# Optimization experiments

Measured on AMD Instinct MI355X. Metric: run time of the kernel, lower is better.

## Reference

```python
import jax, jax.numpy as jnp
import numpy as np

N_EMBD = 1024
N_HEAD = 16
HEAD_SIZE = N_EMBD // N_HEAD
EPS = 1e-5


def layernorm(x, g, b):
    mu = jnp.mean(x, axis=-1, keepdims=True)
    var = jnp.var(x, axis=-1, keepdims=True)
    return (x - mu) * jax.lax.rsqrt(var + EPS) * g + b


def setup_inputs() -> dict:
    key = jax.random.key(0)
    ks = jax.random.split(key, 12)
    s = 0.02
    C = N_EMBD
    return {
        "x": jax.random.normal(ks[0], (2, 2048, C), dtype=jnp.float32),
        "Wq": jax.random.normal(ks[1], (C, C), dtype=jnp.float32) * s,
        "Wk": jax.random.normal(ks[2], (C, C), dtype=jnp.float32) * s,
        "Wv": jax.random.normal(ks[3], (C, C), dtype=jnp.float32) * s,
        "Wo": jax.random.normal(ks[4], (C, C), dtype=jnp.float32) * s,
        "bo": jnp.zeros((C,), dtype=jnp.float32),
        "W1": jax.random.normal(ks[5], (C, 4 * C), dtype=jnp.float32) * s,
        "b1": jnp.zeros((4 * C,), dtype=jnp.float32),
        "W2": jax.random.normal(ks[6], (4 * C, C), dtype=jnp.float32) * s,
        "b2": jnp.zeros((C,), dtype=jnp.float32),
        "ln1_g": jnp.ones((C,), dtype=jnp.float32),
        "ln1_b": jnp.zeros((C,), dtype=jnp.float32),
        "ln2_g": jnp.ones((C,), dtype=jnp.float32),
        "ln2_b": jnp.zeros((C,), dtype=jnp.float32),
    }


def reference(x, Wq, Wk, Wv, Wo, bo, W1, b1, W2, b2, ln1_g, ln1_b, ln2_g, ln2_b):
    B, T, C = x.shape
    H, Dh = N_HEAD, HEAD_SIZE

    # --- self-attention branch ---
    h = layernorm(x, ln1_g, ln1_b)
    q = (h @ Wq).reshape(B, T, H, Dh)
    k = (h @ Wk).reshape(B, T, H, Dh)
    v = (h @ Wv).reshape(B, T, H, Dh)

    # NOTE: original scales by C**-0.5 (n_embd), not head_size**-0.5
    scale = C ** (-0.5)
    scores = jnp.einsum("bqhd,bkhd->bhqk", q, k) * scale  # [B,H,T,T]
    causal = jnp.tril(jnp.ones((T, T), dtype=bool))
    scores = jnp.where(causal, scores, -jnp.inf)
    wei = jax.nn.softmax(scores, axis=-1)
    attn = jnp.einsum("bhqk,bkhd->bqhd", wei, v).reshape(B, T, C)
    x = x + attn @ Wo + bo

    # --- MLP branch ---
    h2 = layernorm(x, ln2_g, ln2_b)
    ff = jax.nn.relu(h2 @ W1 + b1) @ W2 + b2
    return x + ff
```

## Files before the change

### kernel.cpp

```cpp
#include <hip/hip_runtime.h>

typedef unsigned short u16;
typedef __bf16 bf16;
typedef bf16 bf16x8 __attribute__((ext_vector_type(8)));
typedef float f32x4 __attribute__((ext_vector_type(4)));


__device__ __forceinline__ u16 f2bf(float f) {
  bf16 b = (bf16)f;
  return __builtin_bit_cast(u16, b);
}

__device__ __forceinline__ void gll16(void* lds, const void* g) {
  __builtin_amdgcn_global_load_lds((__attribute__((address_space(1))) void*)g,
                                   (__attribute__((address_space(3))) void*)lds,
                                   16, 0, 0);
}

__device__ __forceinline__ f32x4 mfma16(bf16x8 a, bf16x8 b, f32x4 c) {
  return __builtin_amdgcn_mfma_f32_16x16x32_bf16(a, b, c, 0, 0, 0);
}


__global__ __launch_bounds__(256)
void transpose_all(const float* __restrict__ Wq, const float* __restrict__ Wk,
                   const float* __restrict__ Wv, const float* __restrict__ Wo,
                   const float* __restrict__ W1, const float* __restrict__ W2,
                   u16* __restrict__ WqT, u16* __restrict__ WkT,
                   u16* __restrict__ WvT, u16* __restrict__ WoT,
                   u16* __restrict__ W1T, u16* __restrict__ W2T) {
  __shared__ float tile[32][33];
  const int id = blockIdx.x;
  const float* src;
  u16* dst;
  int R, C, t;
  if (id < 4096) {
    const int w = id >> 10;
    t = id & 1023; R = 1024; C = 1024;
    src = w == 0 ? Wq : w == 1 ? Wk : w == 2 ? Wv : Wo;
    dst = w == 0 ? WqT : w == 1 ? WkT : w == 2 ? WvT : WoT;
  } else if (id < 8192) {
    t = id - 4096; R = 1024; C = 4096; src = W1; dst = W1T;
  } else {
    t = id - 8192; R = 4096; C = 1024; src = W2; dst = W2T;
  }
  const int tilesx = C >> 5;
  const int c0 = (t % tilesx) * 32, r0 = (t / tilesx) * 32;
  const int tx = threadIdx.x, ty = threadIdx.y;
#pragma unroll
  for (int i = 0; i < 4; ++i)
    tile[ty + i * 8][tx] = src[(size_t)(r0 + ty + i * 8) * C + c0 + tx];
  __syncthreads();
#pragma unroll
  for (int i = 0; i < 4; ++i)
    dst[(size_t)(c0 + ty + i * 8) * R + r0 + tx] = f2bf(tile[tx][ty + i * 8]);
}


__global__ __launch_bounds__(256)
void ln_kernel(const float* __restrict__ x, const float* __restrict__ g,
               const float* __restrict__ bb, u16* __restrict__ h) {
  const int row = blockIdx.x;
  const int tid = threadIdx.x;
  const float4 xv = ((const float4*)(x + (size_t)row * 1024))[tid];
  float s = xv.x + xv.y + xv.z + xv.w;
  float q = xv.x * xv.x + xv.y * xv.y + xv.z * xv.z + xv.w * xv.w;
#pragma unroll
  for (int m = 1; m < 64; m <<= 1) {
    s += __shfl_xor(s, m);
    q += __shfl_xor(q, m);
  }
  __shared__ float ss[4], qq[4];
  const int wid = tid >> 6, lane = tid & 63;
  if (lane == 0) { ss[wid] = s; qq[wid] = q; }
  __syncthreads();
  s = ss[0] + ss[1] + ss[2] + ss[3];
  q = qq[0] + qq[1] + qq[2] + qq[3];
  const float mean = s * (1.0f / 1024.0f);
  const float var = q * (1.0f / 1024.0f) - mean * mean;
  const float rs = rsqrtf(var + 1e-5f);
  const float4 gv = ((const float4*)g)[tid];
  const float4 bv = ((const float4*)bb)[tid];
  ushort4 o;
  o.x = f2bf((xv.x - mean) * rs * gv.x + bv.x);
  o.y = f2bf((xv.y - mean) * rs * gv.y + bv.y);
  o.z = f2bf((xv.z - mean) * rs * gv.z + bv.z);
  o.w = f2bf((xv.w - mean) * rs * gv.w + bv.w);
  ((ushort4*)(h + (size_t)row * 1024))[tid] = o;
}


__device__ __forceinline__ void xcd_swizzle(int& bx, int& by, int& bz) {
  const int gx = gridDim.x, gy = gridDim.y;
  const int nwg = gx * gy * (int)gridDim.z;
  int flat = (int)blockIdx.x + gx * ((int)blockIdx.y + gy * (int)blockIdx.z);
  flat = (flat & 7) * (nwg >> 3) + (flat >> 3);
  bx = flat % gx;
  const int rem = flat / gx;
  by = rem % gy;
  bz = rem / gy;
}


template <int EPI>
__global__ __launch_bounds__(256)
void gemm_bt(const u16* __restrict__ A, const u16* __restrict__ Bt,
             const float* __restrict__ bias, const float* __restrict__ res,
             void* __restrict__ O, int M, int N, int K) {
  __shared__ __align__(16) u16 Alds[2][128 * 32];
  __shared__ __align__(16) u16 Blds[2][128 * 32];
  const int tid = threadIdx.x;
  const int lane = tid & 63, wid = tid >> 6;
  const int rl = lane & 15, kg = lane >> 4;
  int bx, by, bz;
  xcd_swizzle(bx, by, bz);
  const int m0 = by * 128, n0 = bx * 128;
  f32x4 acc[4][4];
#pragma unroll
  for (int i = 0; i < 4; ++i)
#pragma unroll
    for (int j = 0; j < 4; ++j) acc[i][j] = (f32x4){0.f, 0.f, 0.f, 0.f};
  const int wr = wid >> 1, wc = wid & 1;
  const int c0 = wid * 2, c1 = wid * 2 + 1;
  const int srow0 = c0 * 16 + (lane >> 2);
  const int srow1 = c1 * 16 + (lane >> 2);
  const int skol = (lane & 3) * 8;

#define STAGE_BT(buf, k0)                                                      \
  {                                                                            \
    gll16(Alds[buf] + c0 * 512, A + (size_t)(m0 + srow0) * K + (k0) + skol);   \
    gll16(Alds[buf] + c1 * 512, A + (size_t)(m0 + srow1) * K + (k0) + skol);   \
    gll16(Blds[buf] + c0 * 512, Bt + (size_t)(n0 + srow0) * K + (k0) + skol);  \
    gll16(Blds[buf] + c1 * 512, Bt + (size_t)(n0 + srow1) * K + (k0) + skol);  \
  }

  const int nt = K >> 5;
  STAGE_BT(0, 0);
  STAGE_BT(1, 32);
  for (int t = 0; t < nt; ++t) {
    const int cur = t & 1;
    if (t + 1 < nt)
      asm volatile("s_waitcnt vmcnt(4)" ::: "memory");
    else
      asm volatile("s_waitcnt vmcnt(0)" ::: "memory");
    __builtin_amdgcn_s_barrier();
    bf16x8 af[4], bfr[4];
#pragma unroll
    for (int m = 0; m < 4; ++m)
      af[m] = *(const bf16x8*)(Alds[cur] + (wr * 64 + m * 16 + rl) * 32 + kg * 8);
#pragma unroll
    for (int n = 0; n < 4; ++n)
      bfr[n] = *(const bf16x8*)(Blds[cur] + (wc * 64 + n * 16 + rl) * 32 + kg * 8);
    __builtin_amdgcn_s_setprio(1);
#pragma unroll
    for (int m = 0; m < 4; ++m)
#pragma unroll
      for (int n = 0; n < 4; ++n)
        acc[m][n] = mfma16(af[m], bfr[n], acc[m][n]);
    __builtin_amdgcn_s_setprio(0);
    __builtin_amdgcn_s_barrier();
    if (t + 2 < nt) STAGE_BT(cur, (t + 2) << 5);
  }
#undef STAGE_BT

#pragma unroll
  for (int m = 0; m < 4; ++m) {
#pragma unroll
    for (int n = 0; n < 4; ++n) {
      const int col = n0 + wc * 64 + n * 16 + rl;
      const float bv = bias ? bias[col] : 0.f;
#pragma unroll
      for (int r = 0; r < 4; ++r) {
        const int row = m0 + wr * 64 + m * 16 + kg * 4 + r;
        float v = acc[m][n][r] + bv;
        if (EPI == 1) v = v > 0.f ? v : 0.f;
        ((u16*)O)[(size_t)row * N + col] = f2bf(v);
      }
    }
  }
}


template <int EPI>
__global__ __launch_bounds__(256)
void gemm64(const u16* __restrict__ A, const u16* __restrict__ B0,
            const u16* __restrict__ B1, const u16* __restrict__ B2,
            const float* __restrict__ bias, const float* __restrict__ res,
            void* __restrict__ O0, void* __restrict__ O1, void* __restrict__ O2,
            int M, int N, int K) {
  __shared__ __align__(16) u16 Alds[3][64 * 32];
  __shared__ __align__(16) u16 Blds[3][128 * 32];
  const int tid = threadIdx.x;
  const int lane = tid & 63, wid = tid >> 6;
  const int rl = lane & 15, kg = lane >> 4;
  int bx, by, bz;
  xcd_swizzle(bx, by, bz);
  const u16* Bt = bz == 0 ? B0 : (bz == 1 ? B1 : B2);
  const int m0 = by * 64, n0 = bx * 128;
  f32x4 acc[2][4];
#pragma unroll
  for (int i = 0; i < 2; ++i)
#pragma unroll
    for (int j = 0; j < 4; ++j) acc[i][j] = (f32x4){0.f, 0.f, 0.f, 0.f};
  const int wr = wid >> 1, wc = wid & 1;
  const int srow = lane >> 2, skol = (lane & 3) * 8;
  const int arow = wid * 16 + srow;
  const int brow0 = wid * 32 + srow;
  const int brow1 = wid * 32 + 16 + srow;

#define STAGE_64(buf, k0)                                                      \
  {                                                                            \
    gll16(Alds[buf] + wid * 512, A + (size_t)(m0 + arow) * K + (k0) + skol);   \
    gll16(Blds[buf] + wid * 1024,                                              \
          Bt + (size_t)(n0 + brow0) * K + (k0) + skol);                        \
    gll16(Blds[buf] + wid * 1024 + 512,                                        \
          Bt + (size_t)(n0 + brow1) * K + (k0) + skol);                        \
  }

  const int nt = K >> 5;
  STAGE_64(0, 0);
  STAGE_64(1, 32);
  int cur = 0;
  for (int t = 0; t < nt; ++t) {
    if (t + 1 < nt)
      asm volatile("s_waitcnt vmcnt(3)" ::: "memory");
    else
      asm volatile("s_waitcnt vmcnt(0)" ::: "memory");
    __builtin_amdgcn_s_barrier();
    if (t + 2 < nt) {
      const int nxt = cur >= 1 ? cur - 1 : cur + 2;
      STAGE_64(nxt, (t + 2) << 5);
    }
    bf16x8 af[2], bfr[4];
#pragma unroll
    for (int m = 0; m < 2; ++m)
      af[m] = *(const bf16x8*)(Alds[cur] + (wr * 32 + m * 16 + rl) * 32 + kg * 8);
#pragma unroll
    for (int n = 0; n < 4; ++n)
      bfr[n] = *(const bf16x8*)(Blds[cur] + (wc * 64 + n * 16 + rl) * 32 + kg * 8);
    __builtin_amdgcn_s_setprio(1);
#pragma unroll
    for (int m = 0; m < 2; ++m)
#pragma unroll
      for (int n = 0; n < 4; ++n)
        acc[m][n] = mfma16(af[m], bfr[n], acc[m][n]);
    __builtin_amdgcn_s_setprio(0);
    cur = cur + 1 == 3 ? 0 : cur + 1;
  }
#undef STAGE_64

#pragma unroll
  for (int m = 0; m < 2; ++m) {
#pragma unroll
    for (int n = 0; n < 4; ++n) {
      const int col = n0 + wc * 64 + n * 16 + rl;
      const int row0 = m0 + wr * 32 + m * 16 + kg * 4;
      if (EPI == 3 && bz == 2) {
        u16* vt = (u16*)O2;
        const size_t off =
            ((size_t)((row0 >> 11) * 16 + (col >> 6)) * 64 + (col & 63)) * 2048 +
            (row0 & 2047);
        ushort4 pk = {f2bf(acc[m][n][0]), f2bf(acc[m][n][1]),
                      f2bf(acc[m][n][2]), f2bf(acc[m][n][3])};
        *(ushort4*)(vt + off) = pk;
      } else if (EPI == 3) {
        u16* out = (u16*)(bz == 0 ? O0 : O1);
#pragma unroll
        for (int r = 0; r < 4; ++r)
          out[(size_t)(row0 + r) * N + col] = f2bf(acc[m][n][r]);
      } else {
        const float bv = bias[col];
        float* out = (float*)O0;
#pragma unroll
        for (int r = 0; r < 4; ++r) {
          const int row = row0 + r;
          out[(size_t)row * N + col] =
              acc[m][n][r] + bv + res[(size_t)row * N + col];
        }
      }
    }
  }
}


#define SC2 0.045084220027780106f

__device__ __forceinline__ void attn_range(
    const u16* __restrict__ qg, const u16* __restrict__ kgl,
    const u16* __restrict__ vtb, size_t rowb, int cb, char* plw,
    int rl, int kg, int q0, int kvb, int kve, bool mask_last,
    f32x4 (&ot)[2][4], float (&lrun)[2]) {
  if (kvb >= kve) return;
  const int swz = (rl & 7) << 4;
  bf16x8 qf[2][2];
#pragma unroll
  for (int m = 0; m < 2; ++m) {
    const u16* qp = qg + (rowb + q0 + m * 16 + rl) * 1024 + cb + kg * 8;
    qf[m][0] = *(const bf16x8*)(qp);
    qf[m][1] = *(const bf16x8*)(qp + 32);
  }

  bf16x8 ka[4][2], kb[4][2];
#define LOADK(dst, kvi)                                                        \
  {                                                                            \
    const u16* krow = kgl + (rowb + (kvi) * 64 + rl) * 1024 + cb + kg * 8;     \
    _Pragma("unroll") for (int n = 0; n < 4; ++n) {                            \
      dst[n][0] = *(const bf16x8*)(krow + (size_t)n * 16 * 1024);              \
      dst[n][1] = *(const bf16x8*)(krow + (size_t)n * 16 * 1024 + 32);         \
    }                                                                          \
  }

#define BODY(kf, kvi)                                                          \
  {                                                                            \
    const int kv0 = (kvi) * 64;                                                \
    const u16* vrow = vtb + (size_t)rl * 2048 + kv0 + kg * 8;                  \
    bf16x8 vfr[4][2];                                                          \
    _Pragma("unroll") for (int dt = 0; dt < 4; ++dt) {                         \
      vfr[dt][0] = *(const bf16x8*)(vrow + (size_t)dt * 16 * 2048);            \
      vfr[dt][1] = *(const bf16x8*)(vrow + (size_t)dt * 16 * 2048 + 32);       \
    }                                                                          \
    const bool domask = mask_last && ((kvi) == kve - 1);                       \
    _Pragma("unroll") for (int m = 0; m < 2; ++m) {                            \
      f32x4 s[4];                                                              \
      __builtin_amdgcn_s_setprio(1);                                           \
      _Pragma("unroll") for (int n = 0; n < 4; ++n) {                          \
        f32x4 t = (f32x4){0.f, 0.f, 0.f, 0.f};                                 \
        t = mfma16(kf[n][0], qf[m][0], t);                                     \
        t = mfma16(kf[n][1], qf[m][1], t);                                     \
        s[n] = t;                                                              \
      }                                                                        \
      __builtin_amdgcn_s_setprio(0);                                           \
      if (domask) {                                                            \
        const int qrow = q0 + m * 16 + rl;                                     \
        _Pragma("unroll") for (int n = 0; n < 4; ++n)                          \
            _Pragma("unroll") for (int r = 0; r < 4; ++r) {                    \
          const int tk = kv0 + n * 16 + 4 * kg + r;                            \
          s[n][r] = (tk > qrow) ? -3e38f : s[n][r];                            \
        }                                                                      \
      }                                                                        \
      float ps = 0.f;                                                          \
      _Pragma("unroll") for (int n = 0; n < 4; ++n) {                          \
        const float p0 = exp2f(__builtin_fmaf(s[n][0], SC2, -8.f));            \
        const float p1 = exp2f(__builtin_fmaf(s[n][1], SC2, -8.f));            \
        const float p2 = exp2f(__builtin_fmaf(s[n][2], SC2, -8.f));            \
        const float p3 = exp2f(__builtin_fmaf(s[n][3], SC2, -8.f));            \
        ps += (p0 + p1) + (p2 + p3);                                           \
        ushort4 pk = {f2bf(p0), f2bf(p1), f2bf(p2), f2bf(p3)};                 \
        *(ushort4*)(plw + m * 2048 + ((rl * 128 + n * 32 + kg * 8) ^ swz)) =   \
            pk;                                                                \
      }                                                                        \
      lrun[m] += ps;                                                           \
    }                                                                          \
    _Pragma("unroll") for (int m = 0; m < 2; ++m) {                            \
      const bf16x8 pf0 =                                                       \
          *(const bf16x8*)(plw + m * 2048 + ((rl * 128 + kg * 16) ^ swz));     \
      const bf16x8 pf1 = *(const bf16x8*)(plw + m * 2048 +                     \
                                          ((rl * 128 + 64 + kg * 16) ^ swz));  \
      __builtin_amdgcn_s_setprio(1);                                           \
      _Pragma("unroll") for (int dt = 0; dt < 4; ++dt) {                       \
        ot[m][dt] = mfma16(vfr[dt][0], pf0, ot[m][dt]);                        \
        ot[m][dt] = mfma16(vfr[dt][1], pf1, ot[m][dt]);                        \
      }                                                                        \
      __builtin_amdgcn_s_setprio(0);                                           \
    }                                                                          \
  }

  LOADK(ka, kvb);
  int kv = kvb;
  for (;;) {
    if (kv + 1 < kve) LOADK(kb, kv + 1);
    BODY(ka, kv);
    ++kv;
    if (kv >= kve) break;
    if (kv + 1 < kve) LOADK(ka, kv + 1);
    BODY(kb, kv);
    ++kv;
    if (kv >= kve) break;
  }
#undef LOADK
#undef BODY
}

__global__ __launch_bounds__(128)
void attn_kernel(const u16* __restrict__ qg, const u16* __restrict__ kgl,
                 const u16* __restrict__ vtg, u16* __restrict__ og) {
  const int tid = threadIdx.x, lane = tid & 63, wid = tid >> 6;
  const int rl = lane & 15, kg = lane >> 4;
  const int flat = blockIdx.x;
  const int bh = (flat & 7) * 4 + ((flat >> 3) & 3);
  const int pr = flat >> 5;
  const int jA = pr, jB = 63 - pr;
  const int nA = (jA >> 1) + 1, nB = (jB >> 1) + 1;
  const int a = (nB - nA) >> 1;
  const size_t rowb = (size_t)(bh >> 4) * 2048;
  const int cb = (bh & 15) * 64;
  const u16* vtb = vtg + (size_t)bh * 64 * 2048;

  __shared__ __align__(16) char Pl[2][4096];
  __shared__ __align__(16) float MrgO[2][4][64][4];
  __shared__ float MrgL[2][16];
  char* plw = Pl[wid];

  f32x4 ot[2][4];
  float lrun[2] = {0.f, 0.f};
#pragma unroll
  for (int m = 0; m < 2; ++m)
#pragma unroll
    for (int dt = 0; dt < 4; ++dt) ot[m][dt] = (f32x4){0.f, 0.f, 0.f, 0.f};

  if (wid == 0) {
    attn_range(qg, kgl, vtb, rowb, cb, plw, rl, kg, jA * 32, 0, nA, true,
               ot, lrun);
#pragma unroll
    for (int m = 0; m < 2; ++m) {
      lrun[m] += __shfl_xor(lrun[m], 16);
      lrun[m] += __shfl_xor(lrun[m], 32);
      const float inv = 1.f / lrun[m];
      u16* orow = og + (rowb + jA * 32 + m * 16 + rl) * 1024 + cb;
#pragma unroll
      for (int dt = 0; dt < 4; ++dt) {
        ushort4 ok = {f2bf(ot[m][dt][0] * inv), f2bf(ot[m][dt][1] * inv),
                      f2bf(ot[m][dt][2] * inv), f2bf(ot[m][dt][3] * inv)};
        *(ushort4*)(orow + dt * 16 + 4 * kg) = ok;
      }
      lrun[m] = 0.f;
#pragma unroll
      for (int dt = 0; dt < 4; ++dt) ot[m][dt] = (f32x4){0.f, 0.f, 0.f, 0.f};
    }
    attn_range(qg, kgl, vtb, rowb, cb, plw, rl, kg, jB * 32, 0, a, false,
               ot, lrun);
  } else {
    attn_range(qg, kgl, vtb, rowb, cb, plw, rl, kg, jB * 32, a, nB, true,
               ot, lrun);
#pragma unroll
    for (int m = 0; m < 2; ++m) {
      lrun[m] += __shfl_xor(lrun[m], 16);
      lrun[m] += __shfl_xor(lrun[m], 32);
#pragma unroll
      for (int dt = 0; dt < 4; ++dt)
        *(f32x4*)(&MrgO[m][dt][lane][0]) = ot[m][dt];
      if (kg == 0) MrgL[m][rl] = lrun[m];
    }
  }
  __syncthreads();
  if (wid == 0) {
#pragma unroll
    for (int m = 0; m < 2; ++m) {
      lrun[m] += __shfl_xor(lrun[m], 16);
      lrun[m] += __shfl_xor(lrun[m], 32);
      const float inv = 1.f / (lrun[m] + MrgL[m][rl]);
      u16* orow = og + (rowb + jB * 32 + m * 16 + rl) * 1024 + cb;
#pragma unroll
      for (int dt = 0; dt < 4; ++dt) {
        const f32x4 o1 = *(const f32x4*)(&MrgO[m][dt][lane][0]);
        ushort4 ok;
#pragma unroll
        for (int r = 0; r < 4; ++r)
          ((u16*)&ok)[r] = f2bf((ot[m][dt][r] + o1[r]) * inv);
        *(ushort4*)(orow + dt * 16 + 4 * kg) = ok;
      }
    }
  }
}


extern "C" void kernel_launch(void* const* d_in, const int* in_sizes, int n_in,
                              void* d_out, int out_size, void* d_ws, size_t ws_size,
                              hipStream_t stream) {
  const float* x    = (const float*)d_in[0];
  const float* Wq   = (const float*)d_in[1];
  const float* Wk   = (const float*)d_in[2];
  const float* Wv   = (const float*)d_in[3];
  const float* Wo   = (const float*)d_in[4];
  const float* bo   = (const float*)d_in[5];
  const float* W1   = (const float*)d_in[6];
  const float* b1   = (const float*)d_in[7];
  const float* W2   = (const float*)d_in[8];
  const float* b2   = (const float*)d_in[9];
  const float* ln1g = (const float*)d_in[10];
  const float* ln1b = (const float*)d_in[11];
  const float* ln2g = (const float*)d_in[12];
  const float* ln2b = (const float*)d_in[13];
  float* out = (float*)d_out;

  char* ws = (char*)d_ws;
  const size_t MB = 1024 * 1024;
  u16* WqT  = (u16*)(ws + 0 * MB);
  u16* WkT  = (u16*)(ws + 2 * MB);
  u16* WvT  = (u16*)(ws + 4 * MB);
  u16* WoT  = (u16*)(ws + 6 * MB);
  u16* W1T  = (u16*)(ws + 8 * MB);
  u16* W2T  = (u16*)(ws + 16 * MB);
  u16* h    = (u16*)(ws + 24 * MB);
  u16* q    = (u16*)(ws + 32 * MB);
  u16* k    = (u16*)(ws + 40 * MB);
  u16* vt   = (u16*)(ws + 48 * MB);
  u16* attn = (u16*)(ws + 56 * MB);
  float* x1 = (float*)(ws + 64 * MB);
  u16* ff1  = (u16*)(ws + 32 * MB);

  dim3 tblk(32, 8);
  transpose_all<<<12288, tblk, 0, stream>>>(Wq, Wk, Wv, Wo, W1, W2,
                                            WqT, WkT, WvT, WoT, W1T, W2T);

  ln_kernel<<<4096, 256, 0, stream>>>(x, ln1g, ln1b, h);

  gemm64<3><<<dim3(8, 64, 3), 256, 0, stream>>>(h, WqT, WkT, WvT, nullptr,
                                                nullptr, q, k, vt,
                                                4096, 1024, 1024);

  attn_kernel<<<1024, 128, 0, stream>>>(q, k, vt, attn);

  gemm64<2><<<dim3(8, 64, 1), 256, 0, stream>>>(attn, WoT, WoT, WoT, bo, x,
                                                x1, x1, x1, 4096, 1024, 1024);

  ln_kernel<<<4096, 256, 0, stream>>>(x1, ln2g, ln2b, h);

  gemm_bt<1><<<dim3(32, 32, 1), 256, 0, stream>>>(h, W1T, b1, nullptr, ff1,
                                                  4096, 4096, 1024);

  gemm64<2><<<dim3(8, 64, 1), 256, 0, stream>>>(ff1, W2T, W2T, W2T, b2, x1,
                                                out, out, out, 4096, 1024, 4096);
}
```

Before: 286.7 us.

## Fuse QKV into one 128x128 GEMM and swizzle LDS k-chunks to avoid bank conflicts

New measurement: 267.6 us. 6.7% less time.

```diff
diff --git a/kernel.cpp b/kernel.cpp
--- a/kernel.cpp
+++ b/kernel.cpp
@@ -20,6 +20,7 @@
 __device__ __forceinline__ f32x4 mfma16(bf16x8 a, bf16x8 b, f32x4 c) {
   return __builtin_amdgcn_mfma_f32_16x16x32_bf16(a, b, c, 0, 0, 0);
 }
+
 
 
 __global__ __launch_bounds__(256)
@@ -105,13 +106,15 @@
 template <int EPI>
 __global__ __launch_bounds__(256)
 void gemm_bt(const u16* __restrict__ A, const u16* __restrict__ Bt,
-             const float* __restrict__ bias, const float* __restrict__ res,
-             void* __restrict__ O, int M, int N, int K) {
+             const float* __restrict__ bias,
+             void* __restrict__ O0, void* __restrict__ O1, void* __restrict__ O2,
+             int M, int N, int K) {
   __shared__ __align__(16) u16 Alds[2][128 * 32];
   __shared__ __align__(16) u16 Blds[2][128 * 32];
   const int tid = threadIdx.x;
   const int lane = tid & 63, wid = tid >> 6;
   const int rl = lane & 15, kg = lane >> 4;
+  const int ksw = (rl >> 1) & 3;
   int bx, by, bz;
   xcd_swizzle(bx, by, bz);
   const int m0 = by * 128, n0 = bx * 128;
@@ -124,7 +127,7 @@
   const int c0 = wid * 2, c1 = wid * 2 + 1;
   const int srow0 = c0 * 16 + (lane >> 2);
   const int srow1 = c1 * 16 + (lane >> 2);
-  const int skol = (lane & 3) * 8;
+  const int skol = (((lane & 3) ^ ((lane >> 3) & 3))) * 8;
 
 #define STAGE_BT(buf, k0)                                                      \
   {                                                                            \
@@ -147,10 +150,12 @@
     bf16x8 af[4], bfr[4];
 #pragma unroll
     for (int m = 0; m < 4; ++m)
-      af[m] = *(const bf16x8*)(Alds[cur] + (wr * 64 + m * 16 + rl) * 32 + kg * 8);
+      af[m] = *(const bf16x8*)(Alds[cur] + (wr * 64 + m * 16 + rl) * 32 +
+                               (kg ^ ksw) * 8);
 #pragma unroll
     for (int n = 0; n < 4; ++n)
-      bfr[n] = *(const bf16x8*)(Blds[cur] + (wc * 64 + n * 16 + rl) * 32 + kg * 8);
+      bfr[n] = *(const bf16x8*)(Blds[cur] + (wc * 64 + n * 16 + rl) * 32 +
+                                (kg ^ ksw) * 8);
     __builtin_amdgcn_s_setprio(1);
 #pragma unroll
     for (int m = 0; m < 4; ++m)
@@ -168,34 +173,50 @@
 #pragma unroll
     for (int n = 0; n < 4; ++n) {
       const int col = n0 + wc * 64 + n * 16 + rl;
-      const float bv = bias ? bias[col] : 0.f;
-#pragma unroll
-      for (int r = 0; r < 4; ++r) {
-        const int row = m0 + wr * 64 + m * 16 + kg * 4 + r;
-        float v = acc[m][n][r] + bv;
-        if (EPI == 1) v = v > 0.f ? v : 0.f;
-        ((u16*)O)[(size_t)row * N + col] = f2bf(v);
+      const int row0 = m0 + wr * 64 + m * 16 + kg * 4;
+      if (EPI == 0) {
+        const int seg = col >> 10;
+        const int lc = col & 1023;
+        if (seg == 2) {
+          u16* vt = (u16*)O2;
+          const size_t off =
+              ((size_t)((row0 >> 11) * 16 + (lc >> 6)) * 64 + (lc & 63)) * 2048 +
+              (row0 & 2047);
+          ushort4 pk = {f2bf(acc[m][n][0]), f2bf(acc[m][n][1]),
+                        f2bf(acc[m][n][2]), f2bf(acc[m][n][3])};
+          *(ushort4*)(vt + off) = pk;
+        } else {
+          u16* o = (u16*)(seg == 0 ? O0 : O1);
+#pragma unroll
+          for (int r = 0; r < 4; ++r)
+            o[(size_t)(row0 + r) * 1024 + lc] = f2bf(acc[m][n][r]);
+        }
+      } else {
+        const float bv = bias[col];
+#pragma unroll
+        for (int r = 0; r < 4; ++r) {
+          float v = acc[m][n][r] + bv;
+          v = v > 0.f ? v : 0.f;
+          ((u16*)O0)[(size_t)(row0 + r) * N + col] = f2bf(v);
+        }
       }
     }
   }
 }
 
 
-template <int EPI>
 __global__ __launch_bounds__(256)
-void gemm64(const u16* __restrict__ A, const u16* __restrict__ B0,
-            const u16* __restrict__ B1, const u16* __restrict__ B2,
+void gemm64(const u16* __restrict__ A, const u16* __restrict__ Bt,
             const float* __restrict__ bias, const float* __restrict__ res,
-            void* __restrict__ O0, void* __restrict__ O1, void* __restrict__ O2,
-            int M, int N, int K) {
+            float* __restrict__ O, int M, int N, int K) {
   __shared__ __align__(16) u16 Alds[3][64 * 32];
   __shared__ __align__(16) u16 Blds[3][128 * 32];
   const int tid = threadIdx.x;
   const int lane = tid & 63, wid = tid >> 6;
   const int rl = lane & 15, kg = lane >> 4;
+  const int ksw = (rl >> 1) & 3;
   int bx, by, bz;
   xcd_swizzle(bx, by, bz);
-  const u16* Bt = bz == 0 ? B0 : (bz == 1 ? B1 : B2);
   const int m0 = by * 64, n0 = bx * 128;
   f32x4 acc[2][4];
 #pragma unroll
@@ -203,7 +224,8 @@
 #pragma unroll
     for (int j = 0; j < 4; ++j) acc[i][j] = (f32x4){0.f, 0.f, 0.f, 0.f};
   const int wr = wid >> 1, wc = wid & 1;
-  const int srow = lane >> 2, skol = (lane & 3) * 8;
+  const int srow = lane >> 2;
+  const int skol = (((lane & 3) ^ ((lane >> 3) & 3))) * 8;
   const int arow = wid * 16 + srow;
   const int brow0 = wid * 32 + srow;
   const int brow1 = wid * 32 + 16 + srow;
@@ -234,10 +256,12 @@
     bf16x8 af[2], bfr[4];
 #pragma unroll
     for (int m = 0; m < 2; ++m)
-      af[m] = *(const bf16x8*)(Alds[cur] + (wr * 32 + m * 16 + rl) * 32 + kg * 8);
+      af[m] = *(const bf16x8*)(Alds[cur] + (wr * 32 + m * 16 + rl) * 32 +
+                               (kg ^ ksw) * 8);
 #pragma unroll
     for (int n = 0; n < 4; ++n)
-      bfr[n] = *(const bf16x8*)(Blds[cur] + (wc * 64 + n * 16 + rl) * 32 + kg * 8);
+      bfr[n] = *(const bf16x8*)(Blds[cur] + (wc * 64 + n * 16 + rl) * 32 +
+                                (kg ^ ksw) * 8);
     __builtin_amdgcn_s_setprio(1);
 #pragma unroll
     for (int m = 0; m < 2; ++m)
@@ -255,28 +279,12 @@
     for (int n = 0; n < 4; ++n) {
       const int col = n0 + wc * 64 + n * 16 + rl;
       const int row0 = m0 + wr * 32 + m * 16 + kg * 4;
-      if (EPI == 3 && bz == 2) {
-        u16* vt = (u16*)O2;
-        const size_t off =
-            ((size_t)((row0 >> 11) * 16 + (col >> 6)) * 64 + (col & 63)) * 2048 +
-            (row0 & 2047);
-        ushort4 pk = {f2bf(acc[m][n][0]), f2bf(acc[m][n][1]),
-                      f2bf(acc[m][n][2]), f2bf(acc[m][n][3])};
-        *(ushort4*)(vt + off) = pk;
-      } else if (EPI == 3) {
-        u16* out = (u16*)(bz == 0 ? O0 : O1);
-#pragma unroll
-        for (int r = 0; r < 4; ++r)
-          out[(size_t)(row0 + r) * N + col] = f2bf(acc[m][n][r]);
-      } else {
-        const float bv = bias[col];
-        float* out = (float*)O0;
-#pragma unroll
-        for (int r = 0; r < 4; ++r) {
-          const int row = row0 + r;
-          out[(size_t)row * N + col] =
-              acc[m][n][r] + bv + res[(size_t)row * N + col];
-        }
+      const float bv = bias[col];
+#pragma unroll
+      for (int r = 0; r < 4; ++r) {
+        const int row = row0 + r;
+        O[(size_t)row * N + col] =
+            acc[m][n][r] + bv + res[(size_t)row * N + col];
       }
     }
   }
@@ -486,8 +494,6 @@
   char* ws = (char*)d_ws;
   const size_t MB = 1024 * 1024;
   u16* WqT  = (u16*)(ws + 0 * MB);
-  u16* WkT  = (u16*)(ws + 2 * MB);
-  u16* WvT  = (u16*)(ws + 4 * MB);
   u16* WoT  = (u16*)(ws + 6 * MB);
   u16* W1T  = (u16*)(ws + 8 * MB);
   u16* W2T  = (u16*)(ws + 16 * MB);
@@ -498,6 +504,8 @@
   u16* attn = (u16*)(ws + 56 * MB);
   float* x1 = (float*)(ws + 64 * MB);
   u16* ff1  = (u16*)(ws + 32 * MB);
+  u16* WkT  = WqT + 1024 * 1024;
+  u16* WvT  = WqT + 2 * 1024 * 1024;
 
   dim3 tblk(32, 8);
   transpose_all<<<12288, tblk, 0, stream>>>(Wq, Wk, Wv, Wo, W1, W2,
@@ -505,20 +513,19 @@
 
   ln_kernel<<<4096, 256, 0, stream>>>(x, ln1g, ln1b, h);
 
-  gemm64<3><<<dim3(8, 64, 3), 256, 0, stream>>>(h, WqT, WkT, WvT, nullptr,
-                                                nullptr, q, k, vt,
-                                                4096, 1024, 1024);
+  gemm_bt<0><<<dim3(24, 32), 256, 0, stream>>>(h, WqT, nullptr,
+                                               q, k, vt, 4096, 3072, 1024);
 
   attn_kernel<<<1024, 128, 0, stream>>>(q, k, vt, attn);
 
-  gemm64<2><<<dim3(8, 64, 1), 256, 0, stream>>>(attn, WoT, WoT, WoT, bo, x,
-                                                x1, x1, x1, 4096, 1024, 1024);
+  gemm64<<<dim3(8, 64), 256, 0, stream>>>(attn, WoT, bo, x, x1,
+                                          4096, 1024, 1024);
 
   ln_kernel<<<4096, 256, 0, stream>>>(x1, ln2g, ln2b, h);
 
-  gemm_bt<1><<<dim3(32, 32, 1), 256, 0, stream>>>(h, W1T, b1, nullptr, ff1,
-                                                  4096, 4096, 1024);
-
-  gemm64<2><<<dim3(8, 64, 1), 256, 0, stream>>>(ff1, W2T, W2T, W2T, b2, x1,
-                                                out, out, out, 4096, 1024, 4096);
-}
+  gemm_bt<1><<<dim3(32, 32), 256, 0, stream>>>(h, W1T, b1, ff1, ff1, ff1,
+                                               4096, 4096, 1024);
+
+  gemm64<<<dim3(8, 64), 256, 0, stream>>>(ff1, W2T, b2, x1, out,
+                                          4096, 1024, 4096);
+}
```
